# Kernel tuning notes

Hardware: AMD Instinct MI355X
Metric: run time of the kernel (lower is better)

The kernel has to match this reference:

```python
import jax, jax.numpy as jnp
import numpy as np

DIM = 1024
HEAD_DIM = 64
NUM_HEADS = DIM // HEAD_DIM
SCALE = HEAD_DIM ** -0.5


def setup_inputs() -> dict:
    key = jax.random.key(0)
    ks = jax.random.split(key, 12)
    b, n = 4, 2048
    std = DIM ** -0.5
    inp = {
        'words': jax.random.normal(ks[0], (b, n, DIM), jnp.float32),
        'position': jax.random.normal(ks[1], (b, n, DIM), jnp.float32),
        'conscious': jax.random.normal(ks[2], (b, n, DIM), jnp.float32),
        # projection weights stored as [in, out] (torch Linear W^T)
        'w_wq': jax.random.normal(ks[3], (DIM, DIM), jnp.float32) * std,
        'w_wk': jax.random.normal(ks[4], (DIM, DIM), jnp.float32) * std,
        'w_wv': jax.random.normal(ks[5], (DIM, DIM), jnp.float32) * std,
        'w_pq': jax.random.normal(ks[6], (DIM, DIM), jnp.float32) * std,
        'w_pk': jax.random.normal(ks[7], (DIM, DIM), jnp.float32) * std,
        'w_cq': jax.random.normal(ks[8], (DIM, DIM), jnp.float32) * std,
        'w_ck': jax.random.normal(ks[9], (DIM, DIM), jnp.float32) * std,
        'w_out': jax.random.normal(ks[10], (DIM, DIM), jnp.float32) * std,
        'b_out': jax.random.normal(ks[11], (DIM,), jnp.float32) * 0.01,
    }
    return inp


def _heads(x):
    b, n, _ = x.shape
    return x.reshape(b, n, NUM_HEADS, HEAD_DIM).transpose(0, 2, 1, 3)  # b h n d


def reference(words, position, conscious, w_wq, w_wk, w_wv, w_pq, w_pk, w_cq, w_ck, w_out, b_out):
    # fused multi-source q/k: sum of three projections per source
    q = _heads(words @ w_wq + position @ w_pq + conscious @ w_cq)
    k = _heads(words @ w_wk + position @ w_pk + conscious @ w_ck)
    v = _heads(words @ w_wv)
    sim = jnp.einsum('bhid,bhjd->bhij', q, k) * SCALE
    attn = jax.nn.softmax(sim, axis=-1)
    out = jnp.einsum('bhij,bhjd->bhid', attn, v)
    b, h, n, d = out.shape
    out = out.transpose(0, 2, 1, 3).reshape(b, n, h * d)
    return out @ w_out + b_out
```

## Files before the change

kernel.cpp:

```cpp
#include <hip/hip_runtime.h>
#include <hip/hip_bf16.h>

typedef __bf16 bf16_t;
typedef __attribute__((ext_vector_type(8))) __bf16 bf16x8;
typedef __attribute__((ext_vector_type(4))) float f32x4;
typedef __attribute__((ext_vector_type(16))) float f32x16;

__device__ __forceinline__ void gld_lds16(const void* g, void* l) {
  __builtin_amdgcn_global_load_lds((const __attribute__((address_space(1))) void*)g,
                                   (__attribute__((address_space(3))) void*)l, 16, 0, 0);
}

__global__ __launch_bounds__(256) void cast_concat(
    const float* __restrict__ w, const float* __restrict__ p,
    const float* __restrict__ c, bf16_t* __restrict__ X)
{
  unsigned idx = blockIdx.x * 256u + threadIdx.x;
  unsigned src = idx >> 21;
  unsigned rem = idx & ((1u << 21) - 1);
  unsigned row = rem >> 8;
  unsigned k4  = (rem & 255u) * 4u;
  const float* s = (src == 0) ? w : (src == 1) ? p : c;
  f32x4 v = *(const f32x4*)(s + (size_t)row * 1024 + k4);
  ushort4 u;
  u.x = __builtin_bit_cast(unsigned short, (bf16_t)v[0]);
  u.y = __builtin_bit_cast(unsigned short, (bf16_t)v[1]);
  u.z = __builtin_bit_cast(unsigned short, (bf16_t)v[2]);
  u.w = __builtin_bit_cast(unsigned short, (bf16_t)v[3]);
  *(ushort4*)(X + (size_t)row * 3072 + src * 1024 + k4) = u;
}

__global__ __launch_bounds__(256) void transpose_all(
    const float* __restrict__ w_wq, const float* __restrict__ w_pq,
    const float* __restrict__ w_cq, const float* __restrict__ w_wk,
    const float* __restrict__ w_pk, const float* __restrict__ w_ck,
    const float* __restrict__ w_wv, const float* __restrict__ w_out,
    bf16_t* __restrict__ Wqkt, bf16_t* __restrict__ Wvt, bf16_t* __restrict__ Wot)
{
  __shared__ float t[32][33];
  const int z = blockIdx.z;
  const float* src; bf16_t* dst; int dstride, koff, roff;
  switch (z) {
    case 0: src = w_wq;  dst = Wqkt; dstride = 3072; koff = 0;    roff = 0;    break;
    case 1: src = w_pq;  dst = Wqkt; dstride = 3072; koff = 1024; roff = 0;    break;
    case 2: src = w_cq;  dst = Wqkt; dstride = 3072; koff = 2048; roff = 0;    break;
    case 3: src = w_wk;  dst = Wqkt; dstride = 3072; koff = 0;    roff = 1024; break;
    case 4: src = w_pk;  dst = Wqkt; dstride = 3072; koff = 1024; roff = 1024; break;
    case 5: src = w_ck;  dst = Wqkt; dstride = 3072; koff = 2048; roff = 1024; break;
    case 6: src = w_wv;  dst = Wvt;  dstride = 1024; koff = 0;    roff = 0;    break;
    default: src = w_out; dst = Wot; dstride = 1024; koff = 0;    roff = 0;    break;
  }
  int bx = blockIdx.x, by = blockIdx.y;
  int x = bx * 32 + threadIdx.x;
  int y0 = by * 32;
  for (int i = threadIdx.y; i < 32; i += 8)
    t[i][threadIdx.x] = src[(size_t)(y0 + i) * 1024 + x];
  __syncthreads();
  int n0 = bx * 32;
  for (int i = threadIdx.y; i < 32; i += 8)
    dst[(size_t)(n0 + i + roff) * dstride + koff + y0 + threadIdx.x] =
        (bf16_t)t[threadIdx.x][i];
}

__global__ __launch_bounds__(512, 2) void gemm256_qk(
    const bf16_t* __restrict__ A, int lda,
    const bf16_t* __restrict__ Bt, int K,
    bf16_t* __restrict__ Qo, bf16_t* __restrict__ Ko, float scale, int nbx)
{
  __shared__ bf16_t As[2][256 * 64];
  __shared__ bf16_t Bs[2][256 * 64];

  const int tid = threadIdx.x;
  const int wave = tid >> 6, lane = tid & 63;
  const int wm = wave >> 2, wn = wave & 3;
  const int lrow = lane & 15, lch = lane >> 4;

  const int nwg = gridDim.x, cpx = nwg >> 3;
  const int id  = blockIdx.x;
  const int swz = (id & 7) * cpx + (id >> 3);
  const int mb = swz / nbx, nb = swz % nbx;
  const int m0 = mb * 256, n0 = nb * 256;

  const int srow = tid >> 3, spp = tid & 7;

  auto STAGE_A = [&](int buf, int k0, int h) {
#pragma unroll
    for (int i = 0; i < 2; ++i) {
      int r = h * 128 + i * 64 + srow;
      int gsw = (spp ^ (r & 7)) * 8;
      gld_lds16(A + (size_t)(m0 + r) * lda + k0 + gsw, &As[buf][r * 64 + spp * 8]);
    }
  };
  auto STAGE_B = [&](int buf, int k0, int h) {
#pragma unroll
    for (int i = 0; i < 2; ++i) {
      int r = h * 128 + i * 64 + srow;
      int gsw = (spp ^ (r & 7)) * 8;
      gld_lds16(Bt + (size_t)(n0 + r) * K + k0 + gsw, &Bs[buf][r * 64 + spp * 8]);
    }
  };

  const int NT = K >> 6;
  STAGE_A(0, 0, 0); STAGE_A(0, 0, 1);
  STAGE_B(0, 0, 0); STAGE_B(0, 0, 1);
  STAGE_B(1, 64, 0); STAGE_B(1, 64, 1);
  asm volatile("s_waitcnt vmcnt(4)" ::: "memory");
  asm volatile("s_barrier" ::: "memory");

  f32x4 acc[8][4] = {};

  for (int kt = 0; kt < NT; ++kt) {
    const int cur = kt & 1, nxt = cur ^ 1;
    bf16x8 bfr[4][2];

#pragma unroll
    for (int p = 0; p < 4; ++p) {
      bf16x8 af[2][2];
#pragma unroll
      for (int j = 0; j < 2; ++j)
#pragma unroll
        for (int ks = 0; ks < 2; ++ks) {
          int r = wm * 128 + (p * 2 + j) * 16 + lrow;
          af[j][ks] = *(const bf16x8*)&As[cur][r * 64 + (((ks * 4 + lch) ^ (r & 7)) * 8)];
        }
      if (p == 0) {
#pragma unroll
        for (int n = 0; n < 4; ++n)
#pragma unroll
          for (int ks = 0; ks < 2; ++ks) {
            int r = wn * 64 + n * 16 + lrow;
            bfr[n][ks] = *(const bf16x8*)&Bs[cur][r * 64 + (((ks * 4 + lch) ^ (r & 7)) * 8)];
          }
      }
      if (p == 0 && kt + 1 < NT) STAGE_A(nxt, (kt + 1) * 64, 0);
      if (p == 1 && kt + 1 < NT) STAGE_A(nxt, (kt + 1) * 64, 1);
      if (p == 2 && kt + 2 < NT) STAGE_B(cur, (kt + 2) * 64, 0);
      if (p == 3 && kt + 2 < NT) STAGE_B(cur, (kt + 2) * 64, 1);
      if (p == 3) {
        if (kt + 2 < NT)      asm volatile("s_waitcnt vmcnt(4)" ::: "memory");
        else                  asm volatile("s_waitcnt vmcnt(0)" ::: "memory");
      }
      asm volatile("s_barrier" ::: "memory");
      __builtin_amdgcn_s_setprio(1);
#pragma unroll
      for (int ks = 0; ks < 2; ++ks)
#pragma unroll
        for (int j = 0; j < 2; ++j)
#pragma unroll
          for (int n = 0; n < 4; ++n)
            acc[p * 2 + j][n] = __builtin_amdgcn_mfma_f32_16x16x32_bf16(
                af[j][ks], bfr[n][ks], acc[p * 2 + j][n], 0, 0, 0);
      __builtin_amdgcn_s_setprio(0);
      asm volatile("s_barrier" ::: "memory");
    }
  }

  const int g = lane >> 4, cl = lane & 15;
#pragma unroll
  for (int m = 0; m < 8; ++m) {
    int m_base = m0 + wm * 128 + m * 16 + g * 4;
    int bb = m_base >> 11, nn = m_base & 2047;
#pragma unroll
    for (int n = 0; n < 4; ++n) {
      int col = n0 + wn * 64 + n * 16 + cl;
      bf16_t* dst = (col < 1024) ? Qo : Ko;
      int cc2 = col & 1023;
      float sc = (col < 1024) ? scale : 1.0f;
      int h = cc2 >> 6, d = cc2 & 63;
      size_t base = ((size_t)(bb * 16 + h) * 2048 + nn) * 64 + d;
#pragma unroll
      for (int r = 0; r < 4; ++r)
        dst[base + (size_t)r * 64] = (bf16_t)(acc[m][n][r] * sc);
    }
  }
}

template<int EPI>
__global__ __launch_bounds__(512, 2) void gemm128x256(
    const bf16_t* __restrict__ A, int lda,
    const bf16_t* __restrict__ Bt, int K,
    void* __restrict__ Cout, const float* __restrict__ bias)
{
  __shared__ bf16_t As[2][128 * 64];
  __shared__ bf16_t Bs[2][256 * 64];

  const int tid = threadIdx.x;
  const int wave = tid >> 6, lane = tid & 63;
  const int wm = wave >> 2, wn = wave & 3;
  const int lrow = lane & 15, lch = lane >> 4;

  const int nwg = gridDim.x, cpx = nwg >> 3;
  const int id  = blockIdx.x;
  const int swz = (id & 7) * cpx + (id >> 3);
  const int mb = swz >> 2, nb = swz & 3;
  const int m0 = mb * 128, n0 = nb * 256;

  const int srow = tid >> 3, spp = tid & 7;

  auto STAGE_A = [&](int buf, int k0, int h) {
    int r = h * 64 + srow;
    int gsw = (spp ^ (r & 7)) * 8;
    gld_lds16(A + (size_t)(m0 + r) * lda + k0 + gsw, &As[buf][r * 64 + spp * 8]);
  };
  auto STAGE_B = [&](int buf, int k0, int h) {
#pragma unroll
    for (int i = 0; i < 2; ++i) {
      int r = h * 128 + i * 64 + srow;
      int gsw = (spp ^ (r & 7)) * 8;
      gld_lds16(Bt + (size_t)(n0 + r) * K + k0 + gsw, &Bs[buf][r * 64 + spp * 8]);
    }
  };

  const int NT = K >> 6;
  STAGE_A(0, 0, 0); STAGE_A(0, 0, 1);
  STAGE_B(0, 0, 0); STAGE_B(0, 0, 1);
  STAGE_B(1, 64, 0); STAGE_B(1, 64, 1);
  asm volatile("s_waitcnt vmcnt(4)" ::: "memory");
  asm volatile("s_barrier" ::: "memory");

  f32x4 acc[4][4] = {};

  for (int kt = 0; kt < NT; ++kt) {
    const int cur = kt & 1, nxt = cur ^ 1;
    bf16x8 bfr[4][2];

#pragma unroll
    for (int p = 0; p < 2; ++p) {
      bf16x8 af[2][2];
#pragma unroll
      for (int j = 0; j < 2; ++j)
#pragma unroll
        for (int ks = 0; ks < 2; ++ks) {
          int r = wm * 64 + (p * 2 + j) * 16 + lrow;
          af[j][ks] = *(const bf16x8*)&As[cur][r * 64 + (((ks * 4 + lch) ^ (r & 7)) * 8)];
        }
      if (p == 0) {
#pragma unroll
        for (int n = 0; n < 4; ++n)
#pragma unroll
          for (int ks = 0; ks < 2; ++ks) {
            int r = wn * 64 + n * 16 + lrow;
            bfr[n][ks] = *(const bf16x8*)&Bs[cur][r * 64 + (((ks * 4 + lch) ^ (r & 7)) * 8)];
          }
      }
      if (p == 0 && kt + 1 < NT) { STAGE_A(nxt, (kt + 1) * 64, 0); STAGE_A(nxt, (kt + 1) * 64, 1); }
      if (p == 1 && kt + 2 < NT) { STAGE_B(cur, (kt + 2) * 64, 0); STAGE_B(cur, (kt + 2) * 64, 1); }
      if (p == 1) {
        if (kt + 2 < NT)      asm volatile("s_waitcnt vmcnt(4)" ::: "memory");
        else                  asm volatile("s_waitcnt vmcnt(0)" ::: "memory");
      }
      asm volatile("s_barrier" ::: "memory");
      __builtin_amdgcn_s_setprio(1);
#pragma unroll
      for (int ks = 0; ks < 2; ++ks)
#pragma unroll
        for (int j = 0; j < 2; ++j)
#pragma unroll
          for (int n = 0; n < 4; ++n)
            acc[p * 2 + j][n] = __builtin_amdgcn_mfma_f32_16x16x32_bf16(
                af[j][ks], bfr[n][ks], acc[p * 2 + j][n], 0, 0, 0);
      __builtin_amdgcn_s_setprio(0);
      asm volatile("s_barrier" ::: "memory");
    }
  }

  const int g = lane >> 4, cl = lane & 15;
  if (EPI == 1) {
    bf16_t* Vo = (bf16_t*)Cout;
#pragma unroll
    for (int m = 0; m < 4; ++m) {
      int m_base = m0 + wm * 64 + m * 16 + g * 4;
      int bb = m_base >> 11, nn = m_base & 2047;
#pragma unroll
      for (int n = 0; n < 4; ++n) {
        int col = n0 + wn * 64 + n * 16 + cl;
        int h = col >> 6, d = col & 63;
        ushort4 u;
        u.x = __builtin_bit_cast(unsigned short, (bf16_t)acc[m][n][0]);
        u.y = __builtin_bit_cast(unsigned short, (bf16_t)acc[m][n][1]);
        u.z = __builtin_bit_cast(unsigned short, (bf16_t)acc[m][n][2]);
        u.w = __builtin_bit_cast(unsigned short, (bf16_t)acc[m][n][3]);
        *(ushort4*)(Vo + ((size_t)(bb * 16 + h) * 64 + d) * 2048 + nn) = u;
      }
    }
  } else {
    float* Co = (float*)Cout;
#pragma unroll
    for (int m = 0; m < 4; ++m) {
      int m_base = m0 + wm * 64 + m * 16 + g * 4;
#pragma unroll
      for (int n = 0; n < 4; ++n) {
        int col = n0 + wn * 64 + n * 16 + cl;
        float bv = bias[col];
#pragma unroll
        for (int r = 0; r < 4; ++r)
          Co[(size_t)(m_base + r) * 1024 + col] = acc[m][n][r] + bv;
      }
    }
  }
}

__global__ __launch_bounds__(256, 2) void attn_kernel(
    const bf16_t* __restrict__ Q, const bf16_t* __restrict__ Kb,
    const bf16_t* __restrict__ Vt, bf16_t* __restrict__ O)
{
  __shared__ bf16_t Ks[2][64 * 64];
  __shared__ bf16_t Vs[2][64 * 64];

  const int fid = blockIdx.x;
  const int swz = (fid & 7) * 64 + (fid >> 3);
  const int bh = swz >> 3, qt = swz & 7;
  const int bb = bh >> 4, h = bh & 15;

  const int tid = threadIdx.x, wave = tid >> 6, lane = tid & 63;
  const int lq = lane & 31;
  const int lh = lane >> 5;

  const bf16_t* Qb    = Q  + ((size_t)bh * 2048 + qt * 256) * 64;
  const bf16_t* Kbase = Kb + (size_t)bh * 2048 * 64;
  const bf16_t* Vbase = Vt + (size_t)bh * 64 * 2048;

  const int srow = tid >> 3, spp = tid & 7;

  auto STAGE_K = [&](int buf, int tile) {
#pragma unroll
    for (int i = 0; i < 2; ++i) {
      int r = i * 32 + srow;
      int sg = (spp ^ (r & 7)) * 8;
      gld_lds16(Kbase + (size_t)(tile * 64 + r) * 64 + sg, &Ks[buf][i * 2048 + tid * 8]);
    }
  };
  auto STAGE_V = [&](int buf, int tile) {
#pragma unroll
    for (int i = 0; i < 2; ++i) {
      int r = i * 32 + srow;
      int sg = (spp ^ (r & 7)) * 8;
      gld_lds16(Vbase + (size_t)r * 2048 + tile * 64 + sg, &Vs[buf][i * 2048 + tid * 8]);
    }
  };

  STAGE_K(0, 0); STAGE_V(0, 0); STAGE_K(1, 1);

  bf16x8 qf0[4], qf1[4];
#pragma unroll
  for (int kf = 0; kf < 4; ++kf) {
    qf0[kf] = *(const bf16x8*)(Qb + (size_t)(wave * 64 + lq) * 64 + kf * 16 + lh * 8);
    qf1[kf] = *(const bf16x8*)(Qb + (size_t)(wave * 64 + 32 + lq) * 64 + kf * 16 + lh * 8);
  }

  f32x16 acc0[2] = {}, acc1[2] = {};
  float m0r = -1.0e30f, l0r = 0.f, m1r = -1.0e30f, l1r = 0.f;
  bf16x8 pb0[4], pb1[4];

  auto QKT2 = [&](int tile, f32x16 (&s0)[2], f32x16 (&s1)[2]) {
    const int kb = tile & 1;
#pragma unroll
    for (int nb2 = 0; nb2 < 2; ++nb2) {
      int r = nb2 * 32 + lq;
      f32x16 z0 = {}, z1 = {};
#pragma unroll
      for (int kf = 0; kf < 4; ++kf) {
        bf16x8 ka = *(const bf16x8*)&Ks[kb][r * 64 + (((kf * 2 + lh) ^ (r & 7)) * 8)];
        z0 = __builtin_amdgcn_mfma_f32_32x32x16_bf16(ka, qf0[kf], z0, 0, 0, 0);
        z1 = __builtin_amdgcn_mfma_f32_32x32x16_bf16(ka, qf1[kf], z1, 0, 0, 0);
      }
      s0[nb2] = z0; s1[nb2] = z1;
    }
  };

  auto PV2 = [&](int tile) {
    const int vb = tile & 1;
#pragma unroll
    for (int ks = 0; ks < 4; ++ks)
#pragma unroll
      for (int db = 0; db < 2; ++db) {
        int r = db * 32 + lq;
        bf16x8 va = *(const bf16x8*)&Vs[vb][r * 64 + (((ks * 2 + lh) ^ (r & 7)) * 8)];
        acc0[db] = __builtin_amdgcn_mfma_f32_32x32x16_bf16(va, pb0[ks], acc0[db], 0, 0, 0);
        acc1[db] = __builtin_amdgcn_mfma_f32_32x32x16_bf16(va, pb1[ks], acc1[db], 0, 0, 0);
      }
  };

  auto SOFTMAX = [&](f32x16 (&st)[2], float& mr, float& lr,
                     f32x16 (&ac)[2], bf16x8 (&po)[4]) {
    float tmax = fmaxf(st[0][0], st[0][1]);
#pragma unroll
    for (int nb2 = 0; nb2 < 2; ++nb2)
#pragma unroll
      for (int rg = (nb2 ? 0 : 2); rg < 16; rg += 2)
        tmax = fmaxf(fmaxf(tmax, st[nb2][rg]), st[nb2][rg + 1]);
    tmax = fmaxf(tmax, __shfl_xor(tmax, 32));

    if (!__all(tmax <= mr + 8.0f)) {
      float mnew = fmaxf(mr, tmax);
      float corr = __builtin_amdgcn_exp2f(mr - mnew);
      mr = mnew;
      lr *= corr;
#pragma unroll
      for (int db = 0; db < 2; ++db)
#pragma unroll
        for (int rg = 0; rg < 16; ++rg)
          ac[db][rg] *= corr;
    }

    float sm = 0.f;
#pragma unroll
    for (int nb2 = 0; nb2 < 2; ++nb2)
#pragma unroll
      for (int rg = 0; rg < 16; ++rg) {
        float p = __builtin_amdgcn_exp2f(st[nb2][rg] - mr);
        st[nb2][rg] = p;
        sm += p;
      }
    sm += __shfl_xor(sm, 32);
    lr += sm;

#pragma unroll
    for (int ks = 0; ks < 4; ++ks) {
      const int nb2 = ks >> 1;
      const int R = (ks & 1) * 8;
      unsigned x0, x1, y0, y1;
      asm("v_cvt_pk_bf16_f32 %0, %1, %2" : "=v"(x0) : "v"(st[nb2][R + 0]), "v"(st[nb2][R + 1]));
      asm("v_cvt_pk_bf16_f32 %0, %1, %2" : "=v"(x1) : "v"(st[nb2][R + 2]), "v"(st[nb2][R + 3]));
      asm("v_cvt_pk_bf16_f32 %0, %1, %2" : "=v"(y0) : "v"(st[nb2][R + 4]), "v"(st[nb2][R + 5]));
      asm("v_cvt_pk_bf16_f32 %0, %1, %2" : "=v"(y1) : "v"(st[nb2][R + 6]), "v"(st[nb2][R + 7]));
      asm volatile("v_permlane32_swap_b32 %0, %1" : "+v"(x0), "+v"(y0));
      asm volatile("v_permlane32_swap_b32 %0, %1" : "+v"(x1), "+v"(y1));
      int4 pw;
      pw.x = (int)x0; pw.y = (int)x1; pw.z = (int)y0; pw.w = (int)y1;
      po[ks] = __builtin_bit_cast(bf16x8, pw);
    }
  };

  asm volatile("s_waitcnt vmcnt(0)" ::: "memory");
  __builtin_amdgcn_s_barrier();
  asm volatile("" ::: "memory");
  {
    f32x16 s0[2], s1[2];
    QKT2(0, s0, s1);
    SOFTMAX(s0, m0r, l0r, acc0, pb0);
    SOFTMAX(s1, m1r, l1r, acc1, pb1);
  }
  asm volatile("s_waitcnt lgkmcnt(0)" ::: "memory");
  __builtin_amdgcn_s_barrier();
  asm volatile("" ::: "memory");

  for (int t = 0; t < 32; ++t) {
    if (t < 30)       { STAGE_V((t + 1) & 1, t + 1); STAGE_K(t & 1, t + 2); }
    else if (t == 30) { STAGE_V(1, 31); }
    if (t < 30)       asm volatile("s_waitcnt vmcnt(4)" ::: "memory");
    else if (t == 30) asm volatile("s_waitcnt vmcnt(2)" ::: "memory");
    else              asm volatile("s_waitcnt vmcnt(0)" ::: "memory");
    __builtin_amdgcn_s_barrier();
    asm volatile("" ::: "memory");

    f32x16 s0[2], s1[2];
    __builtin_amdgcn_s_setprio(1);
    if (t < 31) QKT2(t + 1, s0, s1);
    PV2(t);
    __builtin_amdgcn_s_setprio(0);
    if (t < 31) {
      SOFTMAX(s0, m0r, l0r, acc0, pb0);
      SOFTMAX(s1, m1r, l1r, acc1, pb1);
    }

    asm volatile("s_waitcnt lgkmcnt(0)" ::: "memory");
    __builtin_amdgcn_s_barrier();
    asm volatile("" ::: "memory");
  }

  float inv0 = 1.0f / l0r, inv1 = 1.0f / l1r;
#pragma unroll
  for (int qb = 0; qb < 2; ++qb) {
    float inv = qb ? inv1 : inv0;
    int nn = qt * 256 + wave * 64 + qb * 32 + lq;
    size_t obase = ((size_t)bb * 2048 + nn) * 1024 + h * 64;
#pragma unroll
    for (int db = 0; db < 2; ++db)
#pragma unroll
      for (int rr = 0; rr < 4; ++rr) {
        f32x16& a = qb ? acc1[db] : acc0[db];
        ushort4 u;
        u.x = __builtin_bit_cast(unsigned short, (bf16_t)(a[rr * 4 + 0] * inv));
        u.y = __builtin_bit_cast(unsigned short, (bf16_t)(a[rr * 4 + 1] * inv));
        u.z = __builtin_bit_cast(unsigned short, (bf16_t)(a[rr * 4 + 2] * inv));
        u.w = __builtin_bit_cast(unsigned short, (bf16_t)(a[rr * 4 + 3] * inv));
        *(ushort4*)(O + obase + db * 32 + rr * 8 + lh * 4) = u;
      }
  }
}

extern "C" void kernel_launch(void* const* d_in, const int* in_sizes, int n_in,
                              void* d_out, int out_size, void* d_ws, size_t ws_size,
                              hipStream_t stream) {
  const float* words     = (const float*)d_in[0];
  const float* position  = (const float*)d_in[1];
  const float* conscious = (const float*)d_in[2];
  const float* w_wq  = (const float*)d_in[3];
  const float* w_wk  = (const float*)d_in[4];
  const float* w_wv  = (const float*)d_in[5];
  const float* w_pq  = (const float*)d_in[6];
  const float* w_pk  = (const float*)d_in[7];
  const float* w_cq  = (const float*)d_in[8];
  const float* w_ck  = (const float*)d_in[9];
  const float* w_out = (const float*)d_in[10];
  const float* b_out = (const float*)d_in[11];

  char* ws = (char*)d_ws;
  bf16_t* Xcat = (bf16_t*)(ws);
  bf16_t* Wqkt = (bf16_t*)(ws + 50331648);
  bf16_t* Wvt  = (bf16_t*)(ws + 62914560);
  bf16_t* Wot  = (bf16_t*)(ws + 65011712);
  bf16_t* Qb   = (bf16_t*)(ws + 67108864);
  bf16_t* Kbf  = (bf16_t*)(ws + 83886080);
  bf16_t* Vtb  = (bf16_t*)(ws + 100663296);
  bf16_t* Ob   = (bf16_t*)(ws + 117440512);

  cast_concat<<<24576, 256, 0, stream>>>(words, position, conscious, Xcat);

  transpose_all<<<dim3(32, 32, 8), dim3(32, 8), 0, stream>>>(
      w_wq, w_pq, w_cq, w_wk, w_pk, w_ck, w_wv, w_out, Wqkt, Wvt, Wot);

  gemm256_qk<<<256, 512, 0, stream>>>(Xcat, 3072, Wqkt, 3072, Qb, Kbf,
                                      0.125f * 1.44269504f, 8);
  gemm128x256<1><<<256, 512, 0, stream>>>(Xcat, 3072, Wvt, 1024, Vtb, nullptr);

  attn_kernel<<<512, 256, 0, stream>>>(Qb, Kbf, Vtb, Ob);

  gemm128x256<2><<<256, 512, 0, stream>>>(Ob, 1024, Wot, 1024, (float*)d_out, b_out);
}
```

Before: 271.7 us.

## Use four-slot K/V ring buffer to drop per-iteration trailing barrier

K and V shared-memory buffers grow from two to four slots, and K and V for tile t+2 are now staged together two iterations ahead. Because a buffer is no longer overwritten while a slower wave may still read it, the trailing lgkmcnt wait and barrier at the end of each attention iteration are removed, leaving one barrier per iteration. The softmax max and sum reductions are also split into tree and multi-accumulator forms to shorten dependency chains. The attention kernel's shared memory doubles to 64 KB per block, which could lower occupancy if the two-blocks-per-CU target no longer fits.

```diff
diff --git a/kernel.cpp b/kernel.cpp
--- a/kernel.cpp
+++ b/kernel.cpp
@@ -304,8 +304,8 @@
     const bf16_t* __restrict__ Q, const bf16_t* __restrict__ Kb,
     const bf16_t* __restrict__ Vt, bf16_t* __restrict__ O)
 {
-  __shared__ bf16_t Ks[2][64 * 64];
-  __shared__ bf16_t Vs[2][64 * 64];
+  __shared__ bf16_t Ks[4][64 * 64];
+  __shared__ bf16_t Vs[4][64 * 64];
 
   const int fid = blockIdx.x;
   const int swz = (fid & 7) * 64 + (fid >> 3);
@@ -339,7 +339,7 @@
     }
   };
 
-  STAGE_K(0, 0); STAGE_V(0, 0); STAGE_K(1, 1);
+  STAGE_K(0, 0); STAGE_V(0, 0); STAGE_K(1, 1); STAGE_V(1, 1);
 
   bf16x8 qf0[4], qf1[4];
 #pragma unroll
@@ -353,7 +353,7 @@
   bf16x8 pb0[4], pb1[4];
 
   auto QKT2 = [&](int tile, f32x16 (&s0)[2], f32x16 (&s1)[2]) {
-    const int kb = tile & 1;
+    const int kb = tile & 3;
 #pragma unroll
     for (int nb2 = 0; nb2 < 2; ++nb2) {
       int r = nb2 * 32 + lq;
@@ -369,7 +369,7 @@
   };
 
   auto PV2 = [&](int tile) {
-    const int vb = tile & 1;
+    const int vb = tile & 3;
 #pragma unroll
     for (int ks = 0; ks < 4; ++ks)
 #pragma unroll
@@ -383,12 +383,15 @@
 
   auto SOFTMAX = [&](f32x16 (&st)[2], float& mr, float& lr,
                      f32x16 (&ac)[2], bf16x8 (&po)[4]) {
-    float tmax = fmaxf(st[0][0], st[0][1]);
-#pragma unroll
-    for (int nb2 = 0; nb2 < 2; ++nb2)
-#pragma unroll
-      for (int rg = (nb2 ? 0 : 2); rg < 16; rg += 2)
-        tmax = fmaxf(fmaxf(tmax, st[nb2][rg]), st[nb2][rg + 1]);
+    float mx[8];
+#pragma unroll
+    for (int i = 0; i < 8; ++i)
+      mx[i] = fmaxf(fmaxf(st[0][2 * i], st[0][2 * i + 1]),
+                    fmaxf(st[1][2 * i], st[1][2 * i + 1]));
+#pragma unroll
+    for (int i = 0; i < 4; ++i) mx[i] = fmaxf(mx[i], mx[i + 4]);
+    mx[0] = fmaxf(mx[0], mx[2]); mx[1] = fmaxf(mx[1], mx[3]);
+    float tmax = fmaxf(mx[0], mx[1]);
     tmax = fmaxf(tmax, __shfl_xor(tmax, 32));
 
     if (!__all(tmax <= mr + 8.0f)) {
@@ -403,15 +406,20 @@
           ac[db][rg] *= corr;
     }
 
-    float sm = 0.f;
+    float sm0 = 0.f, sm1 = 0.f, sm2 = 0.f, sm3 = 0.f;
 #pragma unroll
     for (int nb2 = 0; nb2 < 2; ++nb2)
 #pragma unroll
-      for (int rg = 0; rg < 16; ++rg) {
-        float p = __builtin_amdgcn_exp2f(st[nb2][rg] - mr);
-        st[nb2][rg] = p;
-        sm += p;
-      }
+      for (int rg = 0; rg < 16; rg += 4) {
+        float p0 = __builtin_amdgcn_exp2f(st[nb2][rg + 0] - mr);
+        float p1 = __builtin_amdgcn_exp2f(st[nb2][rg + 1] - mr);
+        float p2 = __builtin_amdgcn_exp2f(st[nb2][rg + 2] - mr);
+        float p3 = __builtin_amdgcn_exp2f(st[nb2][rg + 3] - mr);
+        st[nb2][rg + 0] = p0; st[nb2][rg + 1] = p1;
+        st[nb2][rg + 2] = p2; st[nb2][rg + 3] = p3;
+        sm0 += p0; sm1 += p1; sm2 += p2; sm3 += p3;
+      }
+    float sm = (sm0 + sm1) + (sm2 + sm3);
     sm += __shfl_xor(sm, 32);
     lr += sm;
 
@@ -441,15 +449,10 @@
     SOFTMAX(s0, m0r, l0r, acc0, pb0);
     SOFTMAX(s1, m1r, l1r, acc1, pb1);
   }
-  asm volatile("s_waitcnt lgkmcnt(0)" ::: "memory");
-  __builtin_amdgcn_s_barrier();
-  asm volatile("" ::: "memory");
 
   for (int t = 0; t < 32; ++t) {
-    if (t < 30)       { STAGE_V((t + 1) & 1, t + 1); STAGE_K(t & 1, t + 2); }
-    else if (t == 30) { STAGE_V(1, 31); }
+    if (t + 2 < 32) { STAGE_K((t + 2) & 3, t + 2); STAGE_V((t + 2) & 3, t + 2); }
     if (t < 30)       asm volatile("s_waitcnt vmcnt(4)" ::: "memory");
-    else if (t == 30) asm volatile("s_waitcnt vmcnt(2)" ::: "memory");
     else              asm volatile("s_waitcnt vmcnt(0)" ::: "memory");
     __builtin_amdgcn_s_barrier();
     asm volatile("" ::: "memory");
@@ -463,10 +466,6 @@
       SOFTMAX(s0, m0r, l0r, acc0, pb0);
       SOFTMAX(s1, m1r, l1r, acc1, pb1);
     }
-
-    asm volatile("s_waitcnt lgkmcnt(0)" ::: "memory");
-    __builtin_amdgcn_s_barrier();
-    asm volatile("" ::: "memory");
   }
 
   float inv0 = 1.0f / l0r, inv1 = 1.0f / l1r;
```

Result: slower. 281.1 us (+3.4%).
